# Kernel optimization log

Hardware: AMD Instinct MI355X
Metric: run time of the kernel (lower is better)

## Reference

```python
import jax, jax.numpy as jnp
import numpy as np

NHEADS = 16
LORA_SCALE = 16.0 / 16.0  # alpha / r


def lora_linear(x, W, b, A, B):
    # base projection + low-rank LoRA path: x@W^T + b + s*(x@A^T)@B^T
    base = jnp.einsum('bse,oe->bso', x, W) + b
    low = jnp.einsum('bse,re->bsr', x, A)  # [B,S,r]
    return base + LORA_SCALE * jnp.einsum('bsr,or->bso', low, B)


def setup_inputs() -> dict:
    key = jax.random.key(0)
    E, R = 1024, 16
    ks = jax.random.split(key, 20)
    d = {'x': jax.random.normal(ks[0], (4, 1024, E), jnp.float32)}
    i = 1
    for p in ('q', 'k', 'v', 'o'):
        d[f'{p}_w'] = jax.random.normal(ks[i], (E, E), jnp.float32) * 0.02; i += 1
        d[f'{p}_b'] = jax.random.normal(ks[i], (E,), jnp.float32) * 0.02; i += 1
        d[f'{p}_la'] = jax.random.normal(ks[i], (R, E), jnp.float32) * 0.02; i += 1
        d[f'{p}_lb'] = jax.random.normal(ks[i], (E, R), jnp.float32) * 0.02; i += 1
    return d


def reference(x, q_w, q_b, q_la, q_lb, k_w, k_b, k_la, k_lb,
              v_w, v_b, v_la, v_lb, o_w, o_b, o_la, o_lb):
    B, S, E = x.shape
    H = NHEADS
    D = E // H
    q = lora_linear(x, q_w, q_b, q_la, q_lb).reshape(B, S, H, D)
    k = lora_linear(x, k_w, k_b, k_la, k_lb).reshape(B, S, H, D)
    v = lora_linear(x, v_w, v_b, v_la, v_lb).reshape(B, S, H, D)
    scores = jnp.einsum('bshd,bthd->bhst', q, k) / jnp.sqrt(jnp.asarray(D, x.dtype))
    attn = jax.nn.softmax(scores, axis=-1)
    ctx = jnp.einsum('bhst,bthd->bshd', attn, v).reshape(B, S, E)
    return lora_linear(ctx, o_w, o_b, o_la, o_lb)
```

## Files before the change

### kernel.cpp

```cpp
#include <hip/hip_runtime.h>
#include <cstdint>


typedef __attribute__((ext_vector_type(8))) short bf16x8;
typedef __attribute__((ext_vector_type(4))) float f32x4;
typedef __attribute__((ext_vector_type(16))) float f32x16;
typedef __attribute__((ext_vector_type(4))) unsigned short u16x4;
typedef __attribute__((ext_vector_type(4))) unsigned int u32x4;

__device__ __forceinline__ short f2bf(float f) {
  unsigned u = __builtin_bit_cast(unsigned, f);
  u += 0x7FFFu + ((u >> 16) & 1u);
  return (short)(u >> 16);
}

typedef __attribute__((address_space(1))) const unsigned int as1_uint;
typedef __attribute__((address_space(3))) unsigned int as3_uint;

__device__ __forceinline__ void gload_lds16(const short* g, const short* l) {
  __builtin_amdgcn_global_load_lds((as1_uint*)g,
      (as3_uint*)(unsigned int)(uintptr_t)l, 16, 0, 0);
}

__device__ __forceinline__ unsigned cvtpk(float lo, float hi) {
  unsigned r;
  asm("v_cvt_pk_bf16_f32 %0, %1, %2" : "=v"(r) : "v"(lo), "v"(hi));
  return r;
}
__device__ __forceinline__ void plswap(unsigned &a, unsigned &b) {
  asm("v_permlane32_swap_b32 %0, %1" : "+v"(a), "+v"(b));
}

__device__ __forceinline__ void build_pfrag(const f32x16 &s, bf16x8 &f0, bf16x8 &f1) {
  unsigned x0 = cvtpk(s[0], s[1]),  x1 = cvtpk(s[2], s[3]);
  unsigned x2 = cvtpk(s[4], s[5]),  x3 = cvtpk(s[6], s[7]);
  plswap(x0, x2); plswap(x1, x3);
  unsigned y0 = cvtpk(s[8], s[9]),  y1 = cvtpk(s[10], s[11]);
  unsigned y2 = cvtpk(s[12], s[13]), y3 = cvtpk(s[14], s[15]);
  plswap(y0, y2); plswap(y1, y3);
  u32x4 a = {x0, x1, x2, x3}, b = {y0, y1, y2, y3};
  f0 = __builtin_bit_cast(bf16x8, a);
  f1 = __builtin_bit_cast(bf16x8, b);
}

__global__ void build_x(const float* __restrict__ x, short* __restrict__ xb) {
  int idx = blockIdx.x * 256 + threadIdx.x;
  f32x4 v = ((const f32x4*)x)[idx];
  u16x4 o;
  o[0] = (unsigned short)f2bf(v[0]);
  o[1] = (unsigned short)f2bf(v[1]);
  o[2] = (unsigned short)f2bf(v[2]);
  o[3] = (unsigned short)f2bf(v[3]);
  ((u16x4*)xb)[idx] = o;
}

__global__ void fold_w(const float* __restrict__ wq, const float* __restrict__ wk,
                       const float* __restrict__ wv, const float* __restrict__ wo,
                       const float* __restrict__ bq, const float* __restrict__ bk,
                       const float* __restrict__ bv, const float* __restrict__ bo,
                       const float* __restrict__ aq, const float* __restrict__ ak,
                       const float* __restrict__ av, const float* __restrict__ ao,
                       short* __restrict__ out) {
  const int p = blockIdx.y;
  const float* W  = (p == 0) ? wq : (p == 1) ? wk : (p == 2) ? wv : wo;
  const float* Bm = (p == 0) ? bq : (p == 1) ? bk : (p == 2) ? bv : bo;
  const float* A  = (p == 0) ? aq : (p == 1) ? ak : (p == 2) ? av : ao;
  const int idx = blockIdx.x * 256 + threadIdx.x;
  const int n = idx >> 8;
  const int e4 = idx & 255;
  f32x4 acc = ((const f32x4*)(W + (size_t)n * 1024))[e4];
  const float* br = Bm + n * 16;
  #pragma unroll
  for (int r = 0; r < 16; ++r) {
    const f32x4 a4 = ((const f32x4*)(A + (size_t)r * 1024))[e4];
    const float b = br[r];
    acc[0] += b * a4[0];
    acc[1] += b * a4[1];
    acc[2] += b * a4[2];
    acc[3] += b * a4[3];
  }
  u16x4 o;
  o[0] = (unsigned short)f2bf(acc[0]);
  o[1] = (unsigned short)f2bf(acc[1]);
  o[2] = (unsigned short)f2bf(acc[2]);
  o[3] = (unsigned short)f2bf(acc[3]);
  *(u16x4*)(out + (size_t)p * 1048576 + (size_t)idx * 4) = o;
}

__global__ __launch_bounds__(512)
void gemm_qkv(const short* __restrict__ xb, const short* __restrict__ wb,
              const float* __restrict__ biasq, const float* __restrict__ biask,
              const float* __restrict__ biasv,
              short* __restrict__ qbuf, short* __restrict__ kbuf, short* __restrict__ vtb) {
  __shared__ short Ah[2][2][8192];
  __shared__ short Bh[2][2][8192];
  const int wg = blockIdx.x;
  const int swz = (wg & 7) * 24 + (wg >> 3);
  const int brow = swz / 12, bcol = swz % 12;
  const int tid = threadIdx.x;
  const int wid = tid >> 6, lane = tid & 63;
  const int wr = wid >> 2, wc = wid & 3;
  const int lrow = lane & 15, lk = lane >> 4;
  const int l8 = lane & 7, lh = lane >> 3;
  const int sl = l8 ^ lh;

  const short* Arow = xb + (size_t)brow * 256 * 1024;
  const short* Brow = wb + (size_t)bcol * 256 * 1024;

#define STAGE_H(DST, SRC, hf, buf, kt)                                         \
  { _Pragma("unroll")                                                          \
    for (int i = 0; i < 2; ++i) {                                              \
      gload_lds16((SRC) + (size_t)((hf) * 128 + (i * 8 + wid) * 8 + lh) * 1024 \
                        + (kt) * 64 + sl * 8,                                  \
                  &DST[buf][hf][(i * 8 + wid) * 512]);                         \
    } }

  const f32x4 fz = {0.f, 0.f, 0.f, 0.f};
  f32x4 acc[8][4];
  #pragma unroll
  for (int a = 0; a < 8; ++a)
    #pragma unroll
    for (int b = 0; b < 4; ++b) acc[a][b] = fz;

  STAGE_H(Ah, Arow, 0, 0, 0)
  STAGE_H(Ah, Arow, 1, 0, 0)
  STAGE_H(Bh, Brow, 0, 0, 0)
  STAGE_H(Bh, Brow, 1, 0, 0)

  const int bhalf = wc >> 1;
  for (int kt = 0; kt < 16; ++kt) {
    const int cur = kt & 1;
    asm volatile("s_waitcnt vmcnt(0)" ::: "memory");
    asm volatile("s_waitcnt lgkmcnt(0)" ::: "memory");
    __builtin_amdgcn_s_barrier();

    bf16x8 bfr[4][2];
    #pragma unroll
    for (int nj = 0; nj < 4; ++nj) {
      const int rr = (wc & 1) * 64 + nj * 16 + lrow;
      #pragma unroll
      for (int kc = 0; kc < 2; ++kc)
        bfr[nj][kc] = *(const bf16x8*)(&Bh[cur][bhalf][rr * 64 + (((kc * 4 + lk) ^ (lrow & 7)) * 8)]);
    }

    #pragma unroll
    for (int q = 0; q < 4; ++q) {
      if (kt < 15) {
        if (q == 0)      STAGE_H(Ah, Arow, 0, cur ^ 1, kt + 1)
        else if (q == 1) STAGE_H(Ah, Arow, 1, cur ^ 1, kt + 1)
        else if (q == 2) STAGE_H(Bh, Brow, 0, cur ^ 1, kt + 1)
        else             STAGE_H(Bh, Brow, 1, cur ^ 1, kt + 1)
      }
      bf16x8 afr[2][2];
      #pragma unroll
      for (int m2 = 0; m2 < 2; ++m2) {
        const int rr = (q * 2 + m2) * 16 + lrow;
        #pragma unroll
        for (int kc = 0; kc < 2; ++kc)
          afr[m2][kc] = *(const bf16x8*)(&Ah[cur][wr][rr * 64 + (((kc * 4 + lk) ^ (lrow & 7)) * 8)]);
      }
      __builtin_amdgcn_s_setprio(1);
      #pragma unroll
      for (int kc = 0; kc < 2; ++kc)
        #pragma unroll
        for (int m2 = 0; m2 < 2; ++m2)
          #pragma unroll
          for (int nj = 0; nj < 4; ++nj)
            acc[q * 2 + m2][nj] = __builtin_amdgcn_mfma_f32_16x16x32_bf16(
                afr[m2][kc], bfr[nj][kc], acc[q * 2 + m2][nj], 0, 0, 0);
      __builtin_amdgcn_s_setprio(0);
    }
  }
#undef STAGE_H

  const int p = bcol >> 2;
  const float* bias = (p == 0) ? biasq : (p == 1) ? biask : biasv;
  const float oscale = (p == 0) ? 0.18033688f : 1.0f;
  const int c0 = (bcol & 3) * 256 + wc * 64;
  float bcv[4];
  #pragma unroll
  for (int nj = 0; nj < 4; ++nj)
    bcv[nj] = bias[c0 + nj * 16 + lrow];

  #pragma unroll
  for (int mi = 0; mi < 8; ++mi) {
    #pragma unroll
    for (int r = 0; r < 4; ++r) {
      const int gr = brow * 256 + wr * 128 + mi * 16 + lk * 4 + r;
      const int bb = gr >> 10, s = gr & 1023;
      #pragma unroll
      for (int nj = 0; nj < 4; ++nj) {
        const int gc = c0 + nj * 16 + lrow;
        const float v = (acc[mi][nj][r] + bcv[nj]) * oscale;
        const int h = gc >> 6, d = gc & 63;
        const int bh = bb * 16 + h;
        if (p == 2)
          vtb[((size_t)bh * 64 + d) * 1024 + s] = f2bf(v);
        else
          ((p == 0) ? qbuf : kbuf)[((size_t)bh * 1024 + s) * 64 + d] = f2bf(v);
      }
    }
  }
}

__device__ __forceinline__ void gemm_core_p3(const short* __restrict__ xrow,
                                             const short* __restrict__ wrow,
                                             short (&As)[3][8192], short (&Bs)[3][8192],
                                             f32x4 (&acc)[4][4]) {
  const int tid = threadIdx.x;
  const int wv = tid >> 6, lane = tid & 63;
  const int wr = wv >> 1, wc = wv & 1;
  const int lrow = lane & 15, lk = lane >> 4;
  const int srow = lane >> 3, sphys = lane & 7;

#define STAGE_G(buf, kt)                                                       \
  {                                                                            \
    _Pragma("unroll")                                                          \
    for (int i = 0; i < 4; ++i) {                                              \
      const int ch = i * 4 + wv;                                               \
      const int row = ch * 8 + srow;                                           \
      const int sl = sphys ^ (row & 7);                                        \
      gload_lds16(xrow + (size_t)row * 1024 + (kt) * 64 + sl * 8, As[buf] + ch * 512); \
      gload_lds16(wrow + (size_t)row * 1024 + (kt) * 64 + sl * 8, Bs[buf] + ch * 512); \
    }                                                                          \
  }

  STAGE_G(0, 0);
  STAGE_G(1, 1);
  int cur = 0;
  for (int kt = 0; kt < 16; ++kt) {
    if (kt < 14) {
      const int nb = (cur == 0) ? 2 : (cur - 1);
      STAGE_G(nb, kt + 2);
      asm volatile("s_waitcnt vmcnt(16)" ::: "memory");
    } else if (kt == 14) {
      asm volatile("s_waitcnt vmcnt(8)" ::: "memory");
    } else {
      asm volatile("s_waitcnt vmcnt(0)" ::: "memory");
    }
    __builtin_amdgcn_s_barrier();

    #pragma unroll
    for (int kc = 0; kc < 2; ++kc) {
      bf16x8 af[4], bw[4];
      #pragma unroll
      for (int mi = 0; mi < 4; ++mi) {
        const int row = wr * 64 + mi * 16 + lrow;
        const int slot = (kc * 4 + lk) ^ (row & 7);
        af[mi] = *(const bf16x8*)(As[cur] + row * 64 + slot * 8);
      }
      #pragma unroll
      for (int nj = 0; nj < 4; ++nj) {
        const int row = wc * 64 + nj * 16 + lrow;
        const int slot = (kc * 4 + lk) ^ (row & 7);
        bw[nj] = *(const bf16x8*)(Bs[cur] + row * 64 + slot * 8);
      }
      #pragma unroll
      for (int mi = 0; mi < 4; ++mi)
        #pragma unroll
        for (int nj = 0; nj < 4; ++nj)
          acc[mi][nj] = __builtin_amdgcn_mfma_f32_16x16x32_bf16(af[mi], bw[nj], acc[mi][nj], 0, 0, 0);
    }

    asm volatile("s_waitcnt lgkmcnt(0)" ::: "memory");
    __builtin_amdgcn_s_barrier();
    cur = (cur == 2) ? 0 : (cur + 1);
  }
#undef STAGE_G
}

__global__ __launch_bounds__(256)
void attn_kernel(const short* __restrict__ qbuf, const short* __restrict__ kbuf,
                 const short* __restrict__ vtb, short* __restrict__ cb) {
  __shared__ short Ks[2][64 * 64];
  __shared__ short Vs[2][64 * 64];
  const int bh = blockIdx.x, qt = blockIdx.y;
  const int tid = threadIdx.x, w = tid >> 6, lane = tid & 63;
  const int l31 = lane & 31, hi = lane >> 5;
  const int srow = lane >> 3, sphys = lane & 7;
  const short* Qp = qbuf + (size_t)bh * 65536;
  const short* Kp = kbuf + (size_t)bh * 65536;
  const short* Vp = vtb + (size_t)bh * 65536;
  const int q0 = qt * 128 + w * 32;

  bf16x8 bq[4];
  #pragma unroll
  for (int kc = 0; kc < 4; ++kc)
    bq[kc] = *(const bf16x8*)(Qp + (size_t)(q0 + l31) * 64 + kc * 16 + hi * 8);

  const f32x16 fz16 = {0.f,0.f,0.f,0.f,0.f,0.f,0.f,0.f,0.f,0.f,0.f,0.f,0.f,0.f,0.f,0.f};
  float m_run = -1e30f, l_run = 0.f;
  f32x16 acc0 = fz16, acc1 = fz16;

  #define STAGE_KV(buf, tt)                                                  \
    {                                                                        \
      const int t0s = (tt) * 64;                                             \
      _Pragma("unroll")                                                      \
      for (int i = 0; i < 2; ++i) {                                          \
        const int ch = i * 4 + w;                                            \
        const int row = ch * 8 + srow;                                       \
        const int sl = sphys ^ (row & 7);                                    \
        gload_lds16(Kp + (size_t)(t0s + row) * 64 + sl * 8, Ks[buf] + ch * 512); \
        gload_lds16(Vp + (size_t)row * 1024 + t0s + sl * 8, Vs[buf] + ch * 512); \
      }                                                                      \
    }

  STAGE_KV(0, 0);
  __syncthreads();

  int cur = 0;
  for (int tt = 0; tt < 16; ++tt) {
    if (tt < 15) STAGE_KV(cur ^ 1, tt + 1);

    f32x16 s0 = fz16, s1 = fz16;
    #pragma unroll
    for (int kc = 0; kc < 4; ++kc) {
      const int slot = (kc * 2 + hi) ^ (l31 & 7);
      const bf16x8 ak0 = *(const bf16x8*)(Ks[cur] + l31 * 64 + slot * 8);
      const bf16x8 ak1 = *(const bf16x8*)(Ks[cur] + (32 + l31) * 64 + slot * 8);
      s0 = __builtin_amdgcn_mfma_f32_32x32x16_bf16(ak0, bq[kc], s0, 0, 0, 0);
      s1 = __builtin_amdgcn_mfma_f32_32x32x16_bf16(ak1, bq[kc], s1, 0, 0, 0);
    }

    float tm = s0[0];
    #pragma unroll
    for (int r = 1; r < 16; ++r) tm = fmaxf(tm, s0[r]);
    #pragma unroll
    for (int r = 0; r < 16; ++r) tm = fmaxf(tm, s1[r]);
    tm = fmaxf(tm, __shfl_xor(tm, 32, 64));
    const float mn = fmaxf(m_run, tm);
    const float alpha = exp2f(m_run - mn);
    m_run = mn;
    float rs = 0.f;
    #pragma unroll
    for (int r = 0; r < 16; ++r) { const float p = exp2f(s0[r] - mn); s0[r] = p; rs += p; }
    #pragma unroll
    for (int r = 0; r < 16; ++r) { const float p = exp2f(s1[r] - mn); s1[r] = p; rs += p; }
    rs += __shfl_xor(rs, 32, 64);
    l_run = l_run * alpha + rs;
    #pragma unroll
    for (int r = 0; r < 16; ++r) { acc0[r] *= alpha; acc1[r] *= alpha; }

    bf16x8 pf[4];
    build_pfrag(s0, pf[0], pf[1]);
    build_pfrag(s1, pf[2], pf[3]);

    #pragma unroll
    for (int kc4 = 0; kc4 < 4; ++kc4) {
      const int slot = (kc4 * 2 + hi) ^ (l31 & 7);
      const bf16x8 av0 = *(const bf16x8*)(Vs[cur] + l31 * 64 + slot * 8);
      const bf16x8 av1 = *(const bf16x8*)(Vs[cur] + (32 + l31) * 64 + slot * 8);
      acc0 = __builtin_amdgcn_mfma_f32_32x32x16_bf16(av0, pf[kc4], acc0, 0, 0, 0);
      acc1 = __builtin_amdgcn_mfma_f32_32x32x16_bf16(av1, pf[kc4], acc1, 0, 0, 0);
    }

    __syncthreads();
    cur ^= 1;
  }

  const int bb = bh >> 4, h = bh & 15;
  const int s = q0 + l31;
  short* crow = cb + (size_t)(bb * 1024 + s) * 1024 + h * 64;
  const float inv = 1.f / l_run;
  #pragma unroll
  for (int rp = 0; rp < 8; ++rp) {
    const int r = rp * 2;
    const int d = (r & 3) + 8 * (r >> 2) + 4 * hi;
    const unsigned p0 = (unsigned)(unsigned short)f2bf(acc0[r] * inv)
                      | ((unsigned)(unsigned short)f2bf(acc0[r + 1] * inv) << 16);
    const unsigned p1 = (unsigned)(unsigned short)f2bf(acc1[r] * inv)
                      | ((unsigned)(unsigned short)f2bf(acc1[r + 1] * inv) << 16);
    *(unsigned*)(crow + d) = p0;
    *(unsigned*)(crow + 32 + d) = p1;
  }
  #undef STAGE_KV
}

__global__ __launch_bounds__(256)
void gemm_o(const short* __restrict__ cb, const short* __restrict__ wo,
            const float* __restrict__ biaso, float* __restrict__ out) {
  __shared__ short As[3][8192];
  __shared__ short Bs[3][8192];
  const int brow = blockIdx.y, bcol = blockIdx.x;
  const f32x4 fz = {0.f, 0.f, 0.f, 0.f};
  f32x4 acc[4][4];
  #pragma unroll
  for (int a = 0; a < 4; ++a)
    #pragma unroll
    for (int b = 0; b < 4; ++b) acc[a][b] = fz;

  gemm_core_p3(cb + (size_t)brow * 128 * 1024, wo + (size_t)bcol * 128 * 1024,
               As, Bs, acc);

  const int tid = threadIdx.x;
  const int wv = tid >> 6, lane = tid & 63;
  const int wr = wv >> 1, wc = wv & 1;
  const int lrow = lane & 15, lk = lane >> 4;
  float bcv[4];
  #pragma unroll
  for (int nj = 0; nj < 4; ++nj)
    bcv[nj] = biaso[bcol * 128 + wc * 64 + nj * 16 + lrow];

  #pragma unroll
  for (int mi = 0; mi < 4; ++mi) {
    #pragma unroll
    for (int r = 0; r < 4; ++r) {
      const int gr = brow * 128 + wr * 64 + mi * 16 + lk * 4 + r;
      #pragma unroll
      for (int nj = 0; nj < 4; ++nj) {
        const int gc = bcol * 128 + wc * 64 + nj * 16 + lrow;
        out[(size_t)gr * 1024 + gc] = acc[mi][nj][r] + bcv[nj];
      }
    }
  }
}

extern "C" void kernel_launch(void* const* d_in, const int* in_sizes, int n_in,
                              void* d_out, int out_size, void* d_ws, size_t ws_size,
                              hipStream_t stream) {
  (void)in_sizes; (void)n_in; (void)out_size; (void)ws_size;
  const float* x   = (const float*)d_in[0];
  const float* qw  = (const float*)d_in[1];
  const float* qb  = (const float*)d_in[2];
  const float* qla = (const float*)d_in[3];
  const float* qlb = (const float*)d_in[4];
  const float* kw  = (const float*)d_in[5];
  const float* kb  = (const float*)d_in[6];
  const float* kla = (const float*)d_in[7];
  const float* klb = (const float*)d_in[8];
  const float* vw  = (const float*)d_in[9];
  const float* vb  = (const float*)d_in[10];
  const float* vla = (const float*)d_in[11];
  const float* vlb = (const float*)d_in[12];
  const float* ow  = (const float*)d_in[13];
  const float* ob  = (const float*)d_in[14];
  const float* ola = (const float*)d_in[15];
  const float* olb = (const float*)d_in[16];

  short* xb   = (short*)d_ws;
  short* wb   = xb + (size_t)4096 * 1024;
  short* qbuf = wb + (size_t)4 * 1024 * 1024;
  short* kbuf = qbuf + (size_t)4194304;
  short* vtb  = kbuf + (size_t)4194304;

  build_x<<<4096, 256, 0, stream>>>(x, xb);
  fold_w<<<dim3(1024, 4), 256, 0, stream>>>(qw, kw, vw, ow, qlb, klb, vlb, olb,
                                            qla, kla, vla, ola, wb);
  gemm_qkv<<<192, 512, 0, stream>>>(xb, wb, qb, kb, vb, qbuf, kbuf, vtb);
  attn_kernel<<<dim3(64, 8), 256, 0, stream>>>(qbuf, kbuf, vtb, xb);
  gemm_o<<<dim3(8, 32), 256, 0, stream>>>(xb, wb + (size_t)3 * 1024 * 1024, ob, (float*)d_out);
}
```

Measured before the change: 132.4 us.

## Merge prep kernels, repipeline QKV GEMM, add lazy softmax rescale and priorities

Merges the x conversion and LoRA weight folding into one prep launch. Restructures the QKV GEMM pipeline: B tiles are prefetched two steps ahead, barriers and waitcnts move to per-quarter points, and launch bounds now request two blocks per CU. In attention, the max and sum reductions become trees, the running max is rescaled only when the new max exceeds the old by more than 8, and MFMA sections get raised wave priority; the output GEMM also gets raised priority around its MFMAs. The finer-grained barriers and the lazy rescale add synchronisation and numeric-range risk in exchange for less stall time and fewer exp/rescale operations.

```diff
diff --git a/kernel.cpp b/kernel.cpp
--- a/kernel.cpp
+++ b/kernel.cpp
@@ -43,51 +43,54 @@
   f1 = __builtin_bit_cast(bf16x8, b);
 }
 
-__global__ void build_x(const float* __restrict__ x, short* __restrict__ xb) {
-  int idx = blockIdx.x * 256 + threadIdx.x;
-  f32x4 v = ((const f32x4*)x)[idx];
-  u16x4 o;
-  o[0] = (unsigned short)f2bf(v[0]);
-  o[1] = (unsigned short)f2bf(v[1]);
-  o[2] = (unsigned short)f2bf(v[2]);
-  o[3] = (unsigned short)f2bf(v[3]);
-  ((u16x4*)xb)[idx] = o;
-}
-
-__global__ void fold_w(const float* __restrict__ wq, const float* __restrict__ wk,
-                       const float* __restrict__ wv, const float* __restrict__ wo,
-                       const float* __restrict__ bq, const float* __restrict__ bk,
-                       const float* __restrict__ bv, const float* __restrict__ bo,
-                       const float* __restrict__ aq, const float* __restrict__ ak,
-                       const float* __restrict__ av, const float* __restrict__ ao,
-                       short* __restrict__ out) {
-  const int p = blockIdx.y;
-  const float* W  = (p == 0) ? wq : (p == 1) ? wk : (p == 2) ? wv : wo;
-  const float* Bm = (p == 0) ? bq : (p == 1) ? bk : (p == 2) ? bv : bo;
-  const float* A  = (p == 0) ? aq : (p == 1) ? ak : (p == 2) ? av : ao;
-  const int idx = blockIdx.x * 256 + threadIdx.x;
-  const int n = idx >> 8;
-  const int e4 = idx & 255;
-  f32x4 acc = ((const f32x4*)(W + (size_t)n * 1024))[e4];
-  const float* br = Bm + n * 16;
-  #pragma unroll
-  for (int r = 0; r < 16; ++r) {
-    const f32x4 a4 = ((const f32x4*)(A + (size_t)r * 1024))[e4];
-    const float b = br[r];
-    acc[0] += b * a4[0];
-    acc[1] += b * a4[1];
-    acc[2] += b * a4[2];
-    acc[3] += b * a4[3];
-  }
-  u16x4 o;
-  o[0] = (unsigned short)f2bf(acc[0]);
-  o[1] = (unsigned short)f2bf(acc[1]);
-  o[2] = (unsigned short)f2bf(acc[2]);
-  o[3] = (unsigned short)f2bf(acc[3]);
-  *(u16x4*)(out + (size_t)p * 1048576 + (size_t)idx * 4) = o;
-}
-
-__global__ __launch_bounds__(512)
+__global__ void prep_kernel(const float* __restrict__ x, short* __restrict__ xb,
+                            const float* __restrict__ wq, const float* __restrict__ wk,
+                            const float* __restrict__ wv, const float* __restrict__ wo,
+                            const float* __restrict__ bq, const float* __restrict__ bk,
+                            const float* __restrict__ bv, const float* __restrict__ bo,
+                            const float* __restrict__ aq, const float* __restrict__ ak,
+                            const float* __restrict__ av, const float* __restrict__ ao,
+                            short* __restrict__ wbo) {
+  const int b = blockIdx.x;
+  if (b < 4096) {
+    const int idx = b * 256 + threadIdx.x;
+    f32x4 v = ((const f32x4*)x)[idx];
+    u16x4 o;
+    o[0] = (unsigned short)f2bf(v[0]);
+    o[1] = (unsigned short)f2bf(v[1]);
+    o[2] = (unsigned short)f2bf(v[2]);
+    o[3] = (unsigned short)f2bf(v[3]);
+    ((u16x4*)xb)[idx] = o;
+  } else {
+    const int bb = b - 4096;
+    const int p = bb >> 10;
+    const float* W  = (p == 0) ? wq : (p == 1) ? wk : (p == 2) ? wv : wo;
+    const float* Bm = (p == 0) ? bq : (p == 1) ? bk : (p == 2) ? bv : bo;
+    const float* A  = (p == 0) ? aq : (p == 1) ? ak : (p == 2) ? av : ao;
+    const int idx = (bb & 1023) * 256 + threadIdx.x;
+    const int n = idx >> 8;
+    const int e4 = idx & 255;
+    f32x4 acc = ((const f32x4*)(W + (size_t)n * 1024))[e4];
+    const float* br = Bm + n * 16;
+    #pragma unroll
+    for (int r = 0; r < 16; ++r) {
+      const f32x4 a4 = ((const f32x4*)(A + (size_t)r * 1024))[e4];
+      const float bl = br[r];
+      acc[0] += bl * a4[0];
+      acc[1] += bl * a4[1];
+      acc[2] += bl * a4[2];
+      acc[3] += bl * a4[3];
+    }
+    u16x4 o;
+    o[0] = (unsigned short)f2bf(acc[0]);
+    o[1] = (unsigned short)f2bf(acc[1]);
+    o[2] = (unsigned short)f2bf(acc[2]);
+    o[3] = (unsigned short)f2bf(acc[3]);
+    *(u16x4*)(wbo + (size_t)p * 1048576 + (size_t)idx * 4) = o;
+  }
+}
+
+__global__ __launch_bounds__(512, 2)
 void gemm_qkv(const short* __restrict__ xb, const short* __restrict__ wb,
               const float* __restrict__ biasq, const float* __restrict__ biask,
               const float* __restrict__ biasv,
@@ -101,18 +104,17 @@
   const int wid = tid >> 6, lane = tid & 63;
   const int wr = wid >> 2, wc = wid & 3;
   const int lrow = lane & 15, lk = lane >> 4;
-  const int l8 = lane & 7, lh = lane >> 3;
-  const int sl = l8 ^ lh;
-
-  const short* Arow = xb + (size_t)brow * 256 * 1024;
-  const short* Brow = wb + (size_t)bcol * 256 * 1024;
-
-#define STAGE_H(DST, SRC, hf, buf, kt)                                         \
+  const int sl8 = (tid & 7) ^ ((tid >> 3) & 7);
+
+  const short* Asrc = xb + (size_t)brow * 256 * 1024;
+  const short* Bsrc = wb + (size_t)bcol * 256 * 1024;
+
+#define STAGE_H(SRC, LDS, hf, kt, buf)                                         \
   { _Pragma("unroll")                                                          \
     for (int i = 0; i < 2; ++i) {                                              \
-      gload_lds16((SRC) + (size_t)((hf) * 128 + (i * 8 + wid) * 8 + lh) * 1024 \
-                        + (kt) * 64 + sl * 8,                                  \
-                  &DST[buf][hf][(i * 8 + wid) * 512]);                         \
+      const int row = (hf) * 128 + i * 64 + (tid >> 3);                        \
+      gload_lds16(SRC + (size_t)row * 1024 + (kt) * 64 + sl8 * 8,              \
+                  LDS[buf][hf] + (i * 64 + wid * 8) * 64);                     \
     } }
 
   const f32x4 fz = {0.f, 0.f, 0.f, 0.f};
@@ -122,43 +124,46 @@
     #pragma unroll
     for (int b = 0; b < 4; ++b) acc[a][b] = fz;
 
-  STAGE_H(Ah, Arow, 0, 0, 0)
-  STAGE_H(Ah, Arow, 1, 0, 0)
-  STAGE_H(Bh, Brow, 0, 0, 0)
-  STAGE_H(Bh, Brow, 1, 0, 0)
+  STAGE_H(Asrc, Ah, 0, 0, 0)
+  STAGE_H(Asrc, Ah, 1, 0, 0)
+  STAGE_H(Bsrc, Bh, 0, 0, 0)
+  STAGE_H(Bsrc, Bh, 1, 0, 0)
+  STAGE_H(Bsrc, Bh, 0, 1, 1)
+  STAGE_H(Bsrc, Bh, 1, 1, 1)
+  asm volatile("s_waitcnt vmcnt(4)" ::: "memory");
+  __builtin_amdgcn_s_barrier();
 
   const int bhalf = wc >> 1;
-  for (int kt = 0; kt < 16; ++kt) {
-    const int cur = kt & 1;
-    asm volatile("s_waitcnt vmcnt(0)" ::: "memory");
-    asm volatile("s_waitcnt lgkmcnt(0)" ::: "memory");
-    __builtin_amdgcn_s_barrier();
-
+  for (int t = 0; t < 16; ++t) {
+    const int cur = t & 1;
     bf16x8 bfr[4][2];
     #pragma unroll
-    for (int nj = 0; nj < 4; ++nj) {
-      const int rr = (wc & 1) * 64 + nj * 16 + lrow;
-      #pragma unroll
-      for (int kc = 0; kc < 2; ++kc)
-        bfr[nj][kc] = *(const bf16x8*)(&Bh[cur][bhalf][rr * 64 + (((kc * 4 + lk) ^ (lrow & 7)) * 8)]);
-    }
-
-    #pragma unroll
     for (int q = 0; q < 4; ++q) {
-      if (kt < 15) {
-        if (q == 0)      STAGE_H(Ah, Arow, 0, cur ^ 1, kt + 1)
-        else if (q == 1) STAGE_H(Ah, Arow, 1, cur ^ 1, kt + 1)
-        else if (q == 2) STAGE_H(Bh, Brow, 0, cur ^ 1, kt + 1)
-        else             STAGE_H(Bh, Brow, 1, cur ^ 1, kt + 1)
+      if (q == 0) {
+        #pragma unroll
+        for (int nj = 0; nj < 4; ++nj) {
+          const int rr = (wc & 1) * 64 + nj * 16 + lrow;
+          #pragma unroll
+          for (int kc = 0; kc < 2; ++kc)
+            bfr[nj][kc] = *(const bf16x8*)(&Bh[cur][bhalf][rr * 64 + (((kc * 4 + lk) ^ (rr & 7)) * 8)]);
+        }
       }
       bf16x8 afr[2][2];
       #pragma unroll
       for (int m2 = 0; m2 < 2; ++m2) {
-        const int rr = (q * 2 + m2) * 16 + lrow;
+        const int rr = q * 32 + m2 * 16 + lrow;
         #pragma unroll
         for (int kc = 0; kc < 2; ++kc)
-          afr[m2][kc] = *(const bf16x8*)(&Ah[cur][wr][rr * 64 + (((kc * 4 + lk) ^ (lrow & 7)) * 8)]);
-      }
+          afr[m2][kc] = *(const bf16x8*)(&Ah[cur][wr][rr * 64 + (((kc * 4 + lk) ^ (rr & 7)) * 8)]);
+      }
+      if (q == 0) { if (t + 1 < 16) STAGE_H(Asrc, Ah, 0, t + 1, cur ^ 1) }
+      else if (q == 1) { if (t + 1 < 16) STAGE_H(Asrc, Ah, 1, t + 1, cur ^ 1) }
+      else if (q == 2) { if (t + 2 < 16) STAGE_H(Bsrc, Bh, 0, t + 2, cur) }
+      else             { if (t + 2 < 16) STAGE_H(Bsrc, Bh, 1, t + 2, cur) }
+
+      if (q == 0) asm volatile("s_waitcnt lgkmcnt(8)" ::: "memory");
+      __builtin_amdgcn_s_barrier();
+      asm volatile("s_waitcnt lgkmcnt(0)" ::: "memory");
       __builtin_amdgcn_s_setprio(1);
       #pragma unroll
       for (int kc = 0; kc < 2; ++kc)
@@ -169,6 +174,11 @@
             acc[q * 2 + m2][nj] = __builtin_amdgcn_mfma_f32_16x16x32_bf16(
                 afr[m2][kc], bfr[nj][kc], acc[q * 2 + m2][nj], 0, 0, 0);
       __builtin_amdgcn_s_setprio(0);
+      if (q == 3) {
+        if (t < 14) asm volatile("s_waitcnt vmcnt(4)" ::: "memory");
+        else        asm volatile("s_waitcnt vmcnt(0)" ::: "memory");
+      }
+      __builtin_amdgcn_s_barrier();
     }
   }
 #undef STAGE_H
@@ -201,72 +211,6 @@
       }
     }
   }
-}
-
-__device__ __forceinline__ void gemm_core_p3(const short* __restrict__ xrow,
-                                             const short* __restrict__ wrow,
-                                             short (&As)[3][8192], short (&Bs)[3][8192],
-                                             f32x4 (&acc)[4][4]) {
-  const int tid = threadIdx.x;
-  const int wv = tid >> 6, lane = tid & 63;
-  const int wr = wv >> 1, wc = wv & 1;
-  const int lrow = lane & 15, lk = lane >> 4;
-  const int srow = lane >> 3, sphys = lane & 7;
-
-#define STAGE_G(buf, kt)                                                       \
-  {                                                                            \
-    _Pragma("unroll")                                                          \
-    for (int i = 0; i < 4; ++i) {                                              \
-      const int ch = i * 4 + wv;                                               \
-      const int row = ch * 8 + srow;                                           \
-      const int sl = sphys ^ (row & 7);                                        \
-      gload_lds16(xrow + (size_t)row * 1024 + (kt) * 64 + sl * 8, As[buf] + ch * 512); \
-      gload_lds16(wrow + (size_t)row * 1024 + (kt) * 64 + sl * 8, Bs[buf] + ch * 512); \
-    }                                                                          \
-  }
-
-  STAGE_G(0, 0);
-  STAGE_G(1, 1);
-  int cur = 0;
-  for (int kt = 0; kt < 16; ++kt) {
-    if (kt < 14) {
-      const int nb = (cur == 0) ? 2 : (cur - 1);
-      STAGE_G(nb, kt + 2);
-      asm volatile("s_waitcnt vmcnt(16)" ::: "memory");
-    } else if (kt == 14) {
-      asm volatile("s_waitcnt vmcnt(8)" ::: "memory");
-    } else {
-      asm volatile("s_waitcnt vmcnt(0)" ::: "memory");
-    }
-    __builtin_amdgcn_s_barrier();
-
-    #pragma unroll
-    for (int kc = 0; kc < 2; ++kc) {
-      bf16x8 af[4], bw[4];
-      #pragma unroll
-      for (int mi = 0; mi < 4; ++mi) {
-        const int row = wr * 64 + mi * 16 + lrow;
-        const int slot = (kc * 4 + lk) ^ (row & 7);
-        af[mi] = *(const bf16x8*)(As[cur] + row * 64 + slot * 8);
-      }
-      #pragma unroll
-      for (int nj = 0; nj < 4; ++nj) {
-        const int row = wc * 64 + nj * 16 + lrow;
-        const int slot = (kc * 4 + lk) ^ (row & 7);
-        bw[nj] = *(const bf16x8*)(Bs[cur] + row * 64 + slot * 8);
-      }
-      #pragma unroll
-      for (int mi = 0; mi < 4; ++mi)
-        #pragma unroll
-        for (int nj = 0; nj < 4; ++nj)
-          acc[mi][nj] = __builtin_amdgcn_mfma_f32_16x16x32_bf16(af[mi], bw[nj], acc[mi][nj], 0, 0, 0);
-    }
-
-    asm volatile("s_waitcnt lgkmcnt(0)" ::: "memory");
-    __builtin_amdgcn_s_barrier();
-    cur = (cur == 2) ? 0 : (cur + 1);
-  }
-#undef STAGE_G
 }
 
 __global__ __launch_bounds__(256)
@@ -313,6 +257,7 @@
     if (tt < 15) STAGE_KV(cur ^ 1, tt + 1);
 
     f32x16 s0 = fz16, s1 = fz16;
+    __builtin_amdgcn_s_setprio(1);
     #pragma unroll
     for (int kc = 0; kc < 4; ++kc) {
       const int slot = (kc * 2 + hi) ^ (l31 & 7);
@@ -321,30 +266,51 @@
       s0 = __builtin_amdgcn_mfma_f32_32x32x16_bf16(ak0, bq[kc], s0, 0, 0, 0);
       s1 = __builtin_amdgcn_mfma_f32_32x32x16_bf16(ak1, bq[kc], s1, 0, 0, 0);
     }
-
-    float tm = s0[0];
-    #pragma unroll
-    for (int r = 1; r < 16; ++r) tm = fmaxf(tm, s0[r]);
-    #pragma unroll
-    for (int r = 0; r < 16; ++r) tm = fmaxf(tm, s1[r]);
+    __builtin_amdgcn_s_setprio(0);
+
+    float t16[16];
+    #pragma unroll
+    for (int r = 0; r < 8; ++r) t16[r] = fmaxf(s0[2 * r], s0[2 * r + 1]);
+    #pragma unroll
+    for (int r = 0; r < 8; ++r) t16[8 + r] = fmaxf(s1[2 * r], s1[2 * r + 1]);
+    #pragma unroll
+    for (int r = 0; r < 8; ++r) t16[r] = fmaxf(t16[r], t16[r + 8]);
+    #pragma unroll
+    for (int r = 0; r < 4; ++r) t16[r] = fmaxf(t16[r], t16[r + 4]);
+    float tm = fmaxf(fmaxf(t16[0], t16[1]), fmaxf(t16[2], t16[3]));
     tm = fmaxf(tm, __shfl_xor(tm, 32, 64));
-    const float mn = fmaxf(m_run, tm);
-    const float alpha = exp2f(m_run - mn);
-    m_run = mn;
-    float rs = 0.f;
-    #pragma unroll
-    for (int r = 0; r < 16; ++r) { const float p = exp2f(s0[r] - mn); s0[r] = p; rs += p; }
-    #pragma unroll
-    for (int r = 0; r < 16; ++r) { const float p = exp2f(s1[r] - mn); s1[r] = p; rs += p; }
+
+    if (__any(tm - m_run > 8.0f)) {
+      const float mn = fmaxf(m_run, tm);
+      const float alpha = exp2f(m_run - mn);
+      m_run = mn;
+      l_run *= alpha;
+      #pragma unroll
+      for (int r = 0; r < 16; ++r) { acc0[r] *= alpha; acc1[r] *= alpha; }
+    }
+
+    float a16[16];
+    #pragma unroll
+    for (int r = 0; r < 16; ++r) { s0[r] = exp2f(s0[r] - m_run); }
+    #pragma unroll
+    for (int r = 0; r < 16; ++r) { s1[r] = exp2f(s1[r] - m_run); }
+    #pragma unroll
+    for (int r = 0; r < 8; ++r) a16[r] = s0[2 * r] + s0[2 * r + 1];
+    #pragma unroll
+    for (int r = 0; r < 8; ++r) a16[8 + r] = s1[2 * r] + s1[2 * r + 1];
+    #pragma unroll
+    for (int r = 0; r < 8; ++r) a16[r] += a16[r + 8];
+    #pragma unroll
+    for (int r = 0; r < 4; ++r) a16[r] += a16[r + 4];
+    float rs = (a16[0] + a16[1]) + (a16[2] + a16[3]);
     rs += __shfl_xor(rs, 32, 64);
-    l_run = l_run * alpha + rs;
-    #pragma unroll
-    for (int r = 0; r < 16; ++r) { acc0[r] *= alpha; acc1[r] *= alpha; }
+    l_run += rs;
 
     bf16x8 pf[4];
     build_pfrag(s0, pf[0], pf[1]);
     build_pfrag(s1, pf[2], pf[3]);
 
+    __builtin_amdgcn_s_setprio(1);
     #pragma unroll
     for (int kc4 = 0; kc4 < 4; ++kc4) {
       const int slot = (kc4 * 2 + hi) ^ (l31 & 7);
@@ -353,6 +319,7 @@
       acc0 = __builtin_amdgcn_mfma_f32_32x32x16_bf16(av0, pf[kc4], acc0, 0, 0, 0);
       acc1 = __builtin_amdgcn_mfma_f32_32x32x16_bf16(av1, pf[kc4], acc1, 0, 0, 0);
     }
+    __builtin_amdgcn_s_setprio(0);
 
     __syncthreads();
     cur ^= 1;
@@ -374,6 +341,74 @@
     *(unsigned*)(crow + 32 + d) = p1;
   }
   #undef STAGE_KV
+}
+
+__device__ __forceinline__ void gemm_core_p3(const short* __restrict__ xrow,
+                                             const short* __restrict__ wrow,
+                                             short (&As)[3][8192], short (&Bs)[3][8192],
+                                             f32x4 (&acc)[4][4]) {
+  const int tid = threadIdx.x;
+  const int wv = tid >> 6, lane = tid & 63;
+  const int wr = wv >> 1, wc = wv & 1;
+  const int lrow = lane & 15, lk = lane >> 4;
+  const int srow = lane >> 3, sphys = lane & 7;
+
+#define STAGE_G(buf, kt)                                                       \
+  {                                                                            \
+    _Pragma("unroll")                                                          \
+    for (int i = 0; i < 4; ++i) {                                              \
+      const int ch = i * 4 + wv;                                               \
+      const int row = ch * 8 + srow;                                           \
+      const int sl = sphys ^ (row & 7);                                        \
+      gload_lds16(xrow + (size_t)row * 1024 + (kt) * 64 + sl * 8, As[buf] + ch * 512); \
+      gload_lds16(wrow + (size_t)row * 1024 + (kt) * 64 + sl * 8, Bs[buf] + ch * 512); \
+    }                                                                          \
+  }
+
+  STAGE_G(0, 0);
+  STAGE_G(1, 1);
+  int cur = 0;
+  for (int kt = 0; kt < 16; ++kt) {
+    if (kt < 14) {
+      const int nb = (cur == 0) ? 2 : (cur - 1);
+      STAGE_G(nb, kt + 2);
+      asm volatile("s_waitcnt vmcnt(16)" ::: "memory");
+    } else if (kt == 14) {
+      asm volatile("s_waitcnt vmcnt(8)" ::: "memory");
+    } else {
+      asm volatile("s_waitcnt vmcnt(0)" ::: "memory");
+    }
+    __builtin_amdgcn_s_barrier();
+
+    #pragma unroll
+    for (int kc = 0; kc < 2; ++kc) {
+      bf16x8 af[4], bw[4];
+      #pragma unroll
+      for (int mi = 0; mi < 4; ++mi) {
+        const int row = wr * 64 + mi * 16 + lrow;
+        const int slot = (kc * 4 + lk) ^ (row & 7);
+        af[mi] = *(const bf16x8*)(As[cur] + row * 64 + slot * 8);
+      }
+      #pragma unroll
+      for (int nj = 0; nj < 4; ++nj) {
+        const int row = wc * 64 + nj * 16 + lrow;
+        const int slot = (kc * 4 + lk) ^ (row & 7);
+        bw[nj] = *(const bf16x8*)(Bs[cur] + row * 64 + slot * 8);
+      }
+      __builtin_amdgcn_s_setprio(1);
+      #pragma unroll
+      for (int mi = 0; mi < 4; ++mi)
+        #pragma unroll
+        for (int nj = 0; nj < 4; ++nj)
+          acc[mi][nj] = __builtin_amdgcn_mfma_f32_16x16x32_bf16(af[mi], bw[nj], acc[mi][nj], 0, 0, 0);
+      __builtin_amdgcn_s_setprio(0);
+    }
+
+    asm volatile("s_waitcnt lgkmcnt(0)" ::: "memory");
+    __builtin_amdgcn_s_barrier();
+    cur = (cur == 2) ? 0 : (cur + 1);
+  }
+#undef STAGE_G
 }
 
 __global__ __launch_bounds__(256)
@@ -443,9 +478,9 @@
   short* kbuf = qbuf + (size_t)4194304;
   short* vtb  = kbuf + (size_t)4194304;
 
-  build_x<<<4096, 256, 0, stream>>>(x, xb);
-  fold_w<<<dim3(1024, 4), 256, 0, stream>>>(qw, kw, vw, ow, qlb, klb, vlb, olb,
-                                            qla, kla, vla, ola, wb);
+  prep_kernel<<<8192, 256, 0, stream>>>(x, xb, qw, kw, vw, ow,
+                                        qlb, klb, vlb, olb,
+                                        qla, kla, vla, ola, wb);
   gemm_qkv<<<192, 512, 0, stream>>>(xb, wb, qb, kb, vb, qbuf, kbuf, vtb);
   attn_kernel<<<dim3(64, 8), 256, 0, stream>>>(qbuf, kbuf, vtb, xb);
   gemm_o<<<dim3(8, 32), 256, 0, stream>>>(xb, wb + (size_t)3 * 1024 * 1024, ob, (float*)d_out);
```

Measured after the change: 130.3 us. No clear change (-1.5%).
